# Kernel tuning notes

Hardware: AMD Instinct MI355X
Metric: run time of the kernel (lower is better)

Reference implementation:

```python
import jax, jax.numpy as jnp
import numpy as np

BS, S, D = 2, 2048, 1024
H = 16
DK = D // H  # 64
ROPE_BASE = 10000.0


def _rope(x):
    # x: [b, s, h, dk]; apply rotary embedding along s with per-pair angles.
    s, d = x.shape[1], x.shape[-1]
    theta = 1.0 / (ROPE_BASE ** (jnp.arange(0, d, 2, dtype=jnp.float32) / d))  # [d/2]
    ang = jnp.arange(s, dtype=jnp.float32)[:, None] * theta[None, :]            # [s, d/2]
    cos = jnp.cos(ang)[None, :, None, :]
    sin = jnp.sin(ang)[None, :, None, :]
    xs = x.reshape(*x.shape[:-1], d // 2, 2)
    x0, x1 = xs[..., 0], xs[..., 1]
    out = jnp.stack([x0 * cos - x1 * sin, x1 * cos + x0 * sin], axis=-1)
    return out.reshape(x.shape)


def setup_inputs() -> dict:
    key = jax.random.key(0)
    ks = jax.random.split(key, 7)
    w = 0.02
    return {
        "Q": jax.random.normal(ks[0], (BS, S, D), dtype=jnp.float32),
        "prev": jax.random.normal(ks[1], (BS, H, S, S), dtype=jnp.float32) * 0.1,
        "Wq": jax.random.normal(ks[2], (D, H * DK), dtype=jnp.float32) * w,
        "bq": jnp.zeros((H * DK,), dtype=jnp.float32),
        "Wk": jax.random.normal(ks[3], (D, H * DK), dtype=jnp.float32) * w,
        "bk": jnp.zeros((H * DK,), dtype=jnp.float32),
        "Wv": jax.random.normal(ks[4], (D, H * DK), dtype=jnp.float32) * w,
        "bv": jnp.zeros((H * DK,), dtype=jnp.float32),
        "Wo": jax.random.normal(ks[5], (H * DK, D), dtype=jnp.float32) * w,
        "bo": jnp.zeros((D,), dtype=jnp.float32),
    }


def reference(Q, prev, Wq, bq, Wk, bk, Wv, bv, Wo, bo):
    bs, s, _ = Q.shape
    scale = DK ** -0.5
    # QKV projections (self-attention: K = V = Q)
    q = (Q @ Wq + bq).reshape(bs, s, H, DK)
    k = (Q @ Wk + bk).reshape(bs, s, H, DK)
    v = (Q @ Wv + bv).reshape(bs, s, H, DK)
    # RoPE on q and k (per-call, matching the torch module)
    q = _rope(q)
    k = _rope(k)
    # scores with residual bias from previous layer
    attn_scores = jnp.einsum("bqhd,bkhd->bhqk", q, k) * scale + prev
    attn_weights = jax.nn.softmax(attn_scores, axis=-1)  # dropout p=0.0
    out = jnp.einsum("bhqk,bkhd->bqhd", attn_weights, v).reshape(bs, s, H * DK)
    out = out @ Wo + bo  # proj dropout p=0.0
    return out, attn_scores
```

## Files before the change

kernel.cpp:

```cpp
#include <hip/hip_runtime.h>
#include <hip/hip_bf16.h>
#include <math.h>
#include <cstdint>

#define S_LEN 2048
#define DKH 64

typedef __attribute__((ext_vector_type(8))) short s16x8;
typedef __attribute__((ext_vector_type(4))) float f32x4;

__device__ __forceinline__ unsigned short f2bf(float f) {
  unsigned int u = __float_as_uint(f);
  return (unsigned short)((u + 0x7fffu + ((u >> 16) & 1u)) >> 16);
}

__device__ __forceinline__ void glds16(const unsigned short* g, unsigned short* l) {
  __builtin_amdgcn_global_load_lds(
      (const __attribute__((address_space(1))) unsigned int*)(uintptr_t)g,
      (__attribute__((address_space(3))) unsigned int*)(uintptr_t)l, 16, 0, 0);
}

__global__ void k_rope_table(float* __restrict__ cosT, float* __restrict__ sinT) {
  int idx = blockIdx.x * 256 + threadIdx.x;
  if (idx >= S_LEN * 32) return;
  int s = idx >> 5, i = idx & 31;
  float theta = powf(10000.0f, -(float)i / 32.0f);
  float ang = (float)s * theta;
  float sv, cv;
  sincosf(ang, &sv, &cv);
  cosT[idx] = cv;
  sinT[idx] = sv;
}

__global__ __launch_bounds__(256) void k_wtrans(const float* __restrict__ W,
                                                unsigned short* __restrict__ WT) {
  __shared__ float t[32][33];
  int n0 = blockIdx.x * 32, k0 = blockIdx.y * 32;
  int tx = threadIdx.x & 31, ty = threadIdx.x >> 5;
#pragma unroll
  for (int p = 0; p < 4; ++p)
    t[ty + p * 8][tx] = W[(size_t)(k0 + ty + p * 8) * 1024 + n0 + tx];
  __syncthreads();
#pragma unroll
  for (int p = 0; p < 4; ++p)
    WT[(size_t)(n0 + ty + p * 8) * 1024 + k0 + tx] = f2bf(t[tx][ty + p * 8]);
}

__global__ __launch_bounds__(256) void k_qconv(const float* __restrict__ Q,
                                               unsigned short* __restrict__ Qbf) {
  int idx = (blockIdx.x * 256 + threadIdx.x) * 8;
  float4 a = *(const float4*)(Q + idx);
  float4 b = *(const float4*)(Q + idx + 4);
  s16x8 o;
  o[0] = (short)f2bf(a.x); o[1] = (short)f2bf(a.y); o[2] = (short)f2bf(a.z); o[3] = (short)f2bf(a.w);
  o[4] = (short)f2bf(b.x); o[5] = (short)f2bf(b.y); o[6] = (short)f2bf(b.z); o[7] = (short)f2bf(b.w);
  *(s16x8*)(Qbf + idx) = o;
}

__global__ __launch_bounds__(256) void k_vtrans(const unsigned short* __restrict__ vl,
                                                unsigned short* __restrict__ vt) {
  __shared__ unsigned short t[64][65];
  int bh = blockIdx.y;
  int s0 = blockIdx.x * 64;
  int tx = threadIdx.x & 3;
  int r = threadIdx.x >> 2;
  const unsigned short* src = vl + (size_t)bh * S_LEN * DKH + (size_t)s0 * DKH;
  s16x8 a = *(const s16x8*)(src + r * 64 + tx * 16);
  s16x8 b = *(const s16x8*)(src + r * 64 + tx * 16 + 8);
#pragma unroll
  for (int j = 0; j < 8; ++j) { t[r][tx * 16 + j] = (unsigned short)a[j]; t[r][tx * 16 + 8 + j] = (unsigned short)b[j]; }
  __syncthreads();
  unsigned short* dst = vt + (size_t)bh * DKH * S_LEN + (size_t)r * S_LEN + s0;
  s16x8 o0, o1;
#pragma unroll
  for (int j = 0; j < 8; ++j) { o0[j] = (short)t[tx * 16 + j][r]; o1[j] = (short)t[tx * 16 + 8 + j][r]; }
  *(s16x8*)(dst + tx * 16) = o0;
  *(s16x8*)(dst + tx * 16 + 8) = o1;
}

__global__ __launch_bounds__(256) void k_qkv(
    const unsigned short* __restrict__ Qbf, const unsigned short* __restrict__ WTqkv,
    const float* __restrict__ bq, const float* __restrict__ bk, const float* __restrict__ bv,
    const float* __restrict__ cosT, const float* __restrict__ sinT,
    unsigned short* __restrict__ ql, unsigned short* __restrict__ kl,
    unsigned short* __restrict__ vl) {
  __shared__ unsigned short As[128 * 64];
  __shared__ unsigned short Bs[128 * 64];
  const int m0 = blockIdx.y * 128, n0 = blockIdx.x * 128;
  const int tid = threadIdx.x, lane = tid & 63, wave = tid >> 6;
  const int wm = (wave >> 1) * 64, wn = (wave & 1) * 64;
  const int lr = lane & 15, lg = lane >> 4;
  const int widx = n0 >> 10;
  const float* bias = widx == 0 ? bq : (widx == 1 ? bk : bv);
  const int lrow = lane >> 3, lcol = (lane & 7) * 8;

  f32x4 acc[4][4] = {};
  for (int k0 = 0; k0 < 1024; k0 += 64) {
    __syncthreads();
#pragma unroll
    for (int i = 0; i < 4; ++i) {
      int chunk = wave * 4 + i;
      glds16(Qbf + (size_t)(m0 + 8 * chunk + lrow) * 1024 + k0 + lcol, &As[chunk * 512]);
      glds16(WTqkv + (size_t)(n0 + 8 * chunk + lrow) * 1024 + k0 + lcol, &Bs[chunk * 512]);
    }
    __syncthreads();
#pragma unroll
    for (int ks = 0; ks < 2; ++ks) {
      s16x8 af[4], bf[4];
#pragma unroll
      for (int i = 0; i < 4; ++i) af[i] = *(const s16x8*)&As[(wm + i * 16 + lr) * 64 + ks * 32 + lg * 8];
#pragma unroll
      for (int i = 0; i < 4; ++i) bf[i] = *(const s16x8*)&Bs[(wn + i * 16 + lr) * 64 + ks * 32 + lg * 8];
#pragma unroll
      for (int mi = 0; mi < 4; ++mi)
#pragma unroll
        for (int ni = 0; ni < 4; ++ni)
          acc[mi][ni] = __builtin_amdgcn_mfma_f32_16x16x32_bf16(af[mi], bf[ni], acc[mi][ni], 0, 0, 0);
    }
  }

#pragma unroll
  for (int ni = 0; ni < 4; ++ni) {
    int n = n0 + wn + ni * 16 + lr;
    int np = n & 1023;
    float bval = bias[np];
    int h = np >> 6, d = np & 63;
    int ia = d >> 1;
#pragma unroll
    for (int mi = 0; mi < 4; ++mi) {
#pragma unroll
      for (int r = 0; r < 4; ++r) {
        int m = m0 + wm + mi * 16 + lg * 4 + r;
        int s = m & 2047, b = m >> 11;
        float val = acc[mi][ni][r] + bval;
        size_t oidx = ((size_t)(b * 16 + h) * 2048 + s) * 64 + d;
        if (widx == 2) {
          vl[oidx] = f2bf(val);
        } else {
          float part = __shfl_xor(val, 1);
          float c = cosT[s * 32 + ia], sn = sinT[s * 32 + ia];
          float outv = (d & 1) ? (val * c + part * sn) : (val * c - part * sn);
          (widx == 0 ? ql : kl)[oidx] = f2bf(outv);
        }
      }
    }
  }
}

__global__ __launch_bounds__(256, 4) void k_attn(
    const unsigned short* __restrict__ ql, const unsigned short* __restrict__ kl,
    const unsigned short* __restrict__ vt, const float* __restrict__ prev,
    float* __restrict__ scores, unsigned short* __restrict__ attn_out) {
  __shared__ unsigned short Ks[2][64 * 64];
  __shared__ unsigned short Vs[2][64 * 64];
  __shared__ unsigned short Ps[4][16 * 64];

  const int bid = blockIdx.x;
  const int xcd = bid & 7, idx = bid >> 3;
  const int bh = xcd * 4 + (idx >> 5);
  const int qb = idx & 31;

  const int tid = threadIdx.x, lane = tid & 63, wave = tid >> 6;
  const int lr = lane & 15, lg = lane >> 4;
  const int qw = qb * 64 + wave * 16;
  const int kr = lane >> 3, kc = lane & 7;

  s16x8 qf[2];
#pragma unroll
  for (int ks = 0; ks < 2; ++ks)
    qf[ks] = *(const s16x8*)(ql + ((size_t)bh * S_LEN + qw + lr) * DKH + ks * 32 + lg * 8);

  f32x4 o[4] = {};
  float m_run[4], l_run[4];
#pragma unroll
  for (int r = 0; r < 4; ++r) { m_run[r] = -1e30f; l_run[r] = 0.f; }

  const float scale = 0.125f;
  const unsigned short* kbase = kl + (size_t)bh * S_LEN * DKH;
  const unsigned short* vbase = vt + (size_t)bh * DKH * S_LEN;
  const float* prevB = prev + (size_t)bh * S_LEN * S_LEN;
  float* scoB = scores + (size_t)bh * S_LEN * S_LEN;
  unsigned short* PsW = &Ps[wave][0];

#pragma unroll
  for (int half = 0; half < 2; ++half) {
    const int rb = wave * 16 + half * 8;
    const int row = rb + kr;
    glds16(kbase + (size_t)row * DKH + ((kc ^ kr) * 8), &Ks[0][rb * 64]);
    glds16(vbase + (size_t)row * S_LEN + ((kc ^ kr) * 8), &Vs[0][rb * 64]);
  }
  asm volatile("s_waitcnt vmcnt(0)" ::: "memory");
  __builtin_amdgcn_s_barrier();

  for (int t = 0; t < 32; ++t) {
    const int cur = t & 1;
    const int kv0 = t * 64;
    const int kvn = ((t + 1) & 31) * 64;

    float pvv[16];
#pragma unroll
    for (int n = 0; n < 4; ++n)
#pragma unroll
      for (int r = 0; r < 4; ++r)
        pvv[n * 4 + r] = __builtin_nontemporal_load(
            prevB + (size_t)(qw + lg * 4 + r) * S_LEN + kv0 + n * 16 + lr);
    __builtin_amdgcn_sched_barrier(0);

#pragma unroll
    for (int half = 0; half < 2; ++half) {
      const int rb = wave * 16 + half * 8;
      const int row = rb + kr;
      glds16(kbase + (size_t)(kvn + row) * DKH + ((kc ^ kr) * 8), &Ks[cur ^ 1][rb * 64]);
      glds16(vbase + (size_t)row * S_LEN + kvn + ((kc ^ kr) * 8), &Vs[cur ^ 1][rb * 64]);
    }
    __builtin_amdgcn_sched_barrier(0);

    f32x4 sc[4];
#pragma unroll
    for (int n = 0; n < 4; ++n) {
      f32x4 a = {};
#pragma unroll
      for (int ks = 0; ks < 2; ++ks) {
        s16x8 kf = *(const s16x8*)((const char*)&Ks[cur][0] + (n * 16 + lr) * 128 +
                                   ((ks * 64 + lg * 16) ^ ((lr & 7) << 4)));
        a = __builtin_amdgcn_mfma_f32_16x16x32_bf16(qf[ks], kf, a, 0, 0, 0);
      }
      sc[n] = a;
    }

    float tmax[4] = {-1e30f, -1e30f, -1e30f, -1e30f};
#pragma unroll
    for (int n = 0; n < 4; ++n) {
      const int col = kv0 + n * 16 + lr;
#pragma unroll
      for (int r = 0; r < 4; ++r) {
        float v = sc[n][r] * scale + pvv[n * 4 + r];
        __builtin_nontemporal_store(v, scoB + (size_t)(qw + lg * 4 + r) * S_LEN + col);
        sc[n][r] = v;
        tmax[r] = fmaxf(tmax[r], v);
      }
    }
#pragma unroll
    for (int mask = 1; mask < 16; mask <<= 1)
#pragma unroll
      for (int r = 0; r < 4; ++r) tmax[r] = fmaxf(tmax[r], __shfl_xor(tmax[r], mask));

#pragma unroll
    for (int r = 0; r < 4; ++r) {
      const float mn = fmaxf(m_run[r], tmax[r]);
      const float al = __expf(m_run[r] - mn);
      m_run[r] = mn;
      l_run[r] *= al;
#pragma unroll
      for (int df = 0; df < 4; ++df) o[df][r] *= al;
    }

#pragma unroll
    for (int n = 0; n < 4; ++n)
#pragma unroll
      for (int r = 0; r < 4; ++r) {
        const float p = __expf(sc[n][r] - m_run[r]);
        l_run[r] += p;
        const int prow = lg * 4 + r;
        *(unsigned short*)((char*)PsW + prow * 128 +
                           ((n * 32 + lr * 2) ^ ((prow & 7) << 4))) = f2bf(p);
      }

    s16x8 pa[2];
#pragma unroll
    for (int ks = 0; ks < 2; ++ks)
      pa[ks] = *(const s16x8*)((const char*)PsW + lr * 128 +
                               ((ks * 64 + lg * 16) ^ ((lr & 7) << 4)));
#pragma unroll
    for (int df = 0; df < 4; ++df) {
#pragma unroll
      for (int ks = 0; ks < 2; ++ks) {
        s16x8 vb = *(const s16x8*)((const char*)&Vs[cur][0] + (df * 16 + lr) * 128 +
                                   ((ks * 64 + lg * 16) ^ ((lr & 7) << 4)));
        o[df] = __builtin_amdgcn_mfma_f32_16x16x32_bf16(pa[ks], vb, o[df], 0, 0, 0);
      }
    }

    asm volatile("s_waitcnt vmcnt(16)" ::: "memory");
    __builtin_amdgcn_s_barrier();
  }

#pragma unroll
  for (int mask = 1; mask < 16; mask <<= 1)
#pragma unroll
    for (int r = 0; r < 4; ++r) l_run[r] += __shfl_xor(l_run[r], mask);
  float inv[4];
#pragma unroll
  for (int r = 0; r < 4; ++r) inv[r] = 1.0f / l_run[r];

  const int b = bh >> 4, h = bh & 15;
#pragma unroll
  for (int df = 0; df < 4; ++df) {
    const int d = df * 16 + lr;
#pragma unroll
    for (int r = 0; r < 4; ++r) {
      const int row = qw + lg * 4 + r;
      attn_out[((size_t)(b * S_LEN + row)) * 1024 + h * 64 + d] = f2bf(o[df][r] * inv[r]);
    }
  }
}

__global__ __launch_bounds__(256) void k_outproj(
    const unsigned short* __restrict__ A, const unsigned short* __restrict__ WoT,
    const float* __restrict__ bo, float* __restrict__ out) {
  __shared__ unsigned short As[128 * 64];
  __shared__ unsigned short Bs[128 * 64];
  const int m0 = blockIdx.y * 128, n0 = blockIdx.x * 128;
  const int tid = threadIdx.x, lane = tid & 63, wave = tid >> 6;
  const int wm = (wave >> 1) * 64, wn = (wave & 1) * 64;
  const int lr = lane & 15, lg = lane >> 4;
  const int lrow = lane >> 3, lcol = (lane & 7) * 8;
  f32x4 acc[4][4] = {};
  for (int k0 = 0; k0 < 1024; k0 += 64) {
    __syncthreads();
#pragma unroll
    for (int i = 0; i < 4; ++i) {
      int chunk = wave * 4 + i;
      glds16(A + (size_t)(m0 + 8 * chunk + lrow) * 1024 + k0 + lcol, &As[chunk * 512]);
      glds16(WoT + (size_t)(n0 + 8 * chunk + lrow) * 1024 + k0 + lcol, &Bs[chunk * 512]);
    }
    __syncthreads();
#pragma unroll
    for (int ks = 0; ks < 2; ++ks) {
      s16x8 af[4], bf[4];
#pragma unroll
      for (int i = 0; i < 4; ++i) af[i] = *(const s16x8*)&As[(wm + i * 16 + lr) * 64 + ks * 32 + lg * 8];
#pragma unroll
      for (int i = 0; i < 4; ++i) bf[i] = *(const s16x8*)&Bs[(wn + i * 16 + lr) * 64 + ks * 32 + lg * 8];
#pragma unroll
      for (int mi = 0; mi < 4; ++mi)
#pragma unroll
        for (int ni = 0; ni < 4; ++ni)
          acc[mi][ni] = __builtin_amdgcn_mfma_f32_16x16x32_bf16(af[mi], bf[ni], acc[mi][ni], 0, 0, 0);
    }
  }
#pragma unroll
  for (int ni = 0; ni < 4; ++ni) {
    int n = n0 + wn + ni * 16 + lr;
    float bv = bo[n];
#pragma unroll
    for (int mi = 0; mi < 4; ++mi)
#pragma unroll
      for (int rr = 0; rr < 4; ++rr) {
        int m = m0 + wm + mi * 16 + lg * 4 + rr;
        out[(size_t)m * 1024 + n] = acc[mi][ni][rr] + bv;
      }
  }
}

extern "C" void kernel_launch(void* const* d_in, const int* in_sizes, int n_in,
                              void* d_out, int out_size, void* d_ws, size_t ws_size,
                              hipStream_t stream) {
  const float* Q = (const float*)d_in[0];
  const float* prev = (const float*)d_in[1];
  const float* Wq = (const float*)d_in[2];
  const float* bq = (const float*)d_in[3];
  const float* Wk = (const float*)d_in[4];
  const float* bk = (const float*)d_in[5];
  const float* Wv = (const float*)d_in[6];
  const float* bv = (const float*)d_in[7];
  const float* Wo = (const float*)d_in[8];
  const float* bo = (const float*)d_in[9];

  float* out = (float*)d_out;
  float* scores = out + (size_t)4194304;

  char* ws = (char*)d_ws;
  float* cosT = (float*)ws;
  float* sinT = cosT + 65536;
  unsigned short* WTqkv = (unsigned short*)(ws + 524288);
  unsigned short* WoT = WTqkv + 3145728;
  unsigned short* ql = WoT + 1048576;
  unsigned short* kl = ql + 4194304;
  unsigned short* vl = kl + 4194304;
  unsigned short* vt = vl + 4194304;
  unsigned short* attn_out = vt + 4194304;
  unsigned short* Qbf = attn_out + 4194304;

  k_rope_table<<<256, 256, 0, stream>>>(cosT, sinT);
  k_wtrans<<<dim3(32, 32), 256, 0, stream>>>(Wq, WTqkv);
  k_wtrans<<<dim3(32, 32), 256, 0, stream>>>(Wk, WTqkv + 1048576);
  k_wtrans<<<dim3(32, 32), 256, 0, stream>>>(Wv, WTqkv + 2097152);
  k_wtrans<<<dim3(32, 32), 256, 0, stream>>>(Wo, WoT);
  k_qconv<<<2048, 256, 0, stream>>>(Q, Qbf);
  k_qkv<<<dim3(24, 32), 256, 0, stream>>>(Qbf, WTqkv, bq, bk, bv, cosT, sinT, ql, kl, vl);
  k_vtrans<<<dim3(32, 32), 256, 0, stream>>>(vl, vt);
  k_attn<<<1024, 256, 0, stream>>>(ql, kl, vt, prev, scores, attn_out);
  k_outproj<<<dim3(8, 32), 256, 0, stream>>>(attn_out, WoT, bo, out);
}
```

Before: 384.8 us.

## Widen attention KV tile, read V directly into registers, merge weight transposes, shrink outproj tiles

The attention kernel now processes 128 keys per iteration, which halves the loop trips and barriers. It drops the LDS staging of V and instead loads V fragments straight from global memory into registers, with occupancy lowered to 3 waves per SIMD. The four weight-transpose launches are merged into one 3D-grid kernel. The output projection moves to 64x64 tiles so more blocks run in parallel. The exchange is higher register pressure and uncoalesced per-wave global V reads that every wave repeats, with no LDS sharing of V.

Result: slower. 510.9 us (+32.8%).

```diff
diff --git a/kernel.cpp b/kernel.cpp
--- a/kernel.cpp
+++ b/kernel.cpp
@@ -14,7 +14,7 @@
   return (unsigned short)((u + 0x7fffu + ((u >> 16) & 1u)) >> 16);
 }
 
-__device__ __forceinline__ void glds16(const unsigned short* g, unsigned short* l) {
+__device__ __forceinline__ void glds16(const void* g, void* l) {
   __builtin_amdgcn_global_load_lds(
       (const __attribute__((address_space(1))) unsigned int*)(uintptr_t)g,
       (__attribute__((address_space(3))) unsigned int*)(uintptr_t)l, 16, 0, 0);
@@ -32,9 +32,14 @@
   sinT[idx] = sv;
 }
 
-__global__ __launch_bounds__(256) void k_wtrans(const float* __restrict__ W,
-                                                unsigned short* __restrict__ WT) {
+__global__ __launch_bounds__(256) void k_wtrans4(const float* __restrict__ W0,
+                                                 const float* __restrict__ W1,
+                                                 const float* __restrict__ W2,
+                                                 const float* __restrict__ W3,
+                                                 unsigned short* __restrict__ WT) {
   __shared__ float t[32][33];
+  const float* W = blockIdx.z == 0 ? W0 : (blockIdx.z == 1 ? W1 : (blockIdx.z == 2 ? W2 : W3));
+  unsigned short* dst = WT + (size_t)blockIdx.z * 1048576;
   int n0 = blockIdx.x * 32, k0 = blockIdx.y * 32;
   int tx = threadIdx.x & 31, ty = threadIdx.x >> 5;
 #pragma unroll
@@ -43,7 +48,7 @@
   __syncthreads();
 #pragma unroll
   for (int p = 0; p < 4; ++p)
-    WT[(size_t)(n0 + ty + p * 8) * 1024 + k0 + tx] = f2bf(t[tx][ty + p * 8]);
+    dst[(size_t)(n0 + ty + p * 8) * 1024 + k0 + tx] = f2bf(t[tx][ty + p * 8]);
 }
 
 __global__ __launch_bounds__(256) void k_qconv(const float* __restrict__ Q,
@@ -147,13 +152,12 @@
   }
 }
 
-__global__ __launch_bounds__(256, 4) void k_attn(
+__global__ __launch_bounds__(256, 3) void k_attn(
     const unsigned short* __restrict__ ql, const unsigned short* __restrict__ kl,
     const unsigned short* __restrict__ vt, const float* __restrict__ prev,
     float* __restrict__ scores, unsigned short* __restrict__ attn_out) {
-  __shared__ unsigned short Ks[2][64 * 64];
-  __shared__ unsigned short Vs[2][64 * 64];
-  __shared__ unsigned short Ps[4][16 * 64];
+  __shared__ unsigned short Ks[2][128 * 64];
+  __shared__ unsigned short Ps[4][16 * 128];
 
   const int bid = blockIdx.x;
   const int xcd = bid & 7, idx = bid >> 3;
@@ -183,23 +187,22 @@
   unsigned short* PsW = &Ps[wave][0];
 
 #pragma unroll
-  for (int half = 0; half < 2; ++half) {
-    const int rb = wave * 16 + half * 8;
+  for (int half = 0; half < 4; ++half) {
+    const int rb = wave * 32 + half * 8;
     const int row = rb + kr;
     glds16(kbase + (size_t)row * DKH + ((kc ^ kr) * 8), &Ks[0][rb * 64]);
-    glds16(vbase + (size_t)row * S_LEN + ((kc ^ kr) * 8), &Vs[0][rb * 64]);
   }
   asm volatile("s_waitcnt vmcnt(0)" ::: "memory");
   __builtin_amdgcn_s_barrier();
 
-  for (int t = 0; t < 32; ++t) {
+  for (int t = 0; t < 16; ++t) {
     const int cur = t & 1;
-    const int kv0 = t * 64;
-    const int kvn = ((t + 1) & 31) * 64;
-
-    float pvv[16];
-#pragma unroll
-    for (int n = 0; n < 4; ++n)
+    const int kv0 = t * 128;
+    const int kvn = ((t + 1) & 15) * 128;
+
+    float pvv[32];
+#pragma unroll
+    for (int n = 0; n < 8; ++n)
 #pragma unroll
       for (int r = 0; r < 4; ++r)
         pvv[n * 4 + r] = __builtin_nontemporal_load(
@@ -207,17 +210,25 @@
     __builtin_amdgcn_sched_barrier(0);
 
 #pragma unroll
-    for (int half = 0; half < 2; ++half) {
-      const int rb = wave * 16 + half * 8;
+    for (int half = 0; half < 4; ++half) {
+      const int rb = wave * 32 + half * 8;
       const int row = rb + kr;
       glds16(kbase + (size_t)(kvn + row) * DKH + ((kc ^ kr) * 8), &Ks[cur ^ 1][rb * 64]);
-      glds16(vbase + (size_t)row * S_LEN + kvn + ((kc ^ kr) * 8), &Vs[cur ^ 1][rb * 64]);
     }
     __builtin_amdgcn_sched_barrier(0);
 
-    f32x4 sc[4];
-#pragma unroll
-    for (int n = 0; n < 4; ++n) {
+    s16x8 vf1[8];
+#pragma unroll
+    for (int df = 0; df < 4; ++df)
+#pragma unroll
+      for (int ks = 0; ks < 2; ++ks)
+        vf1[df * 2 + ks] =
+            *(const s16x8*)(vbase + (size_t)(df * 16 + lr) * S_LEN + kv0 + ks * 32 + lg * 8);
+    __builtin_amdgcn_sched_barrier(0);
+
+    f32x4 sc[8];
+#pragma unroll
+    for (int n = 0; n < 8; ++n) {
       f32x4 a = {};
 #pragma unroll
       for (int ks = 0; ks < 2; ++ks) {
@@ -230,7 +241,7 @@
 
     float tmax[4] = {-1e30f, -1e30f, -1e30f, -1e30f};
 #pragma unroll
-    for (int n = 0; n < 4; ++n) {
+    for (int n = 0; n < 8; ++n) {
       const int col = kv0 + n * 16 + lr;
 #pragma unroll
       for (int r = 0; r < 4; ++r) {
@@ -240,6 +251,16 @@
         tmax[r] = fmaxf(tmax[r], v);
       }
     }
+
+    s16x8 vf2[8];
+#pragma unroll
+    for (int df = 0; df < 4; ++df)
+#pragma unroll
+      for (int ks = 0; ks < 2; ++ks)
+        vf2[df * 2 + ks] =
+            *(const s16x8*)(vbase + (size_t)(df * 16 + lr) * S_LEN + kv0 + (ks + 2) * 32 + lg * 8);
+    __builtin_amdgcn_sched_barrier(0);
+
 #pragma unroll
     for (int mask = 1; mask < 16; mask <<= 1)
 #pragma unroll
@@ -256,32 +277,29 @@
     }
 
 #pragma unroll
-    for (int n = 0; n < 4; ++n)
+    for (int n = 0; n < 8; ++n)
 #pragma unroll
       for (int r = 0; r < 4; ++r) {
         const float p = __expf(sc[n][r] - m_run[r]);
         l_run[r] += p;
         const int prow = lg * 4 + r;
-        *(unsigned short*)((char*)PsW + prow * 128 +
+        *(unsigned short*)((char*)PsW + prow * 256 +
                            ((n * 32 + lr * 2) ^ ((prow & 7) << 4))) = f2bf(p);
       }
 
-    s16x8 pa[2];
-#pragma unroll
-    for (int ks = 0; ks < 2; ++ks)
-      pa[ks] = *(const s16x8*)((const char*)PsW + lr * 128 +
+    s16x8 pa[4];
+#pragma unroll
+    for (int ks = 0; ks < 4; ++ks)
+      pa[ks] = *(const s16x8*)((const char*)PsW + lr * 256 +
                                ((ks * 64 + lg * 16) ^ ((lr & 7) << 4)));
 #pragma unroll
     for (int df = 0; df < 4; ++df) {
-#pragma unroll
-      for (int ks = 0; ks < 2; ++ks) {
-        s16x8 vb = *(const s16x8*)((const char*)&Vs[cur][0] + (df * 16 + lr) * 128 +
-                                   ((ks * 64 + lg * 16) ^ ((lr & 7) << 4)));
-        o[df] = __builtin_amdgcn_mfma_f32_16x16x32_bf16(pa[ks], vb, o[df], 0, 0, 0);
-      }
-    }
-
-    asm volatile("s_waitcnt vmcnt(16)" ::: "memory");
+      o[df] = __builtin_amdgcn_mfma_f32_16x16x32_bf16(pa[0], vf1[df * 2 + 0], o[df], 0, 0, 0);
+      o[df] = __builtin_amdgcn_mfma_f32_16x16x32_bf16(pa[1], vf1[df * 2 + 1], o[df], 0, 0, 0);
+      o[df] = __builtin_amdgcn_mfma_f32_16x16x32_bf16(pa[2], vf2[df * 2 + 0], o[df], 0, 0, 0);
+      o[df] = __builtin_amdgcn_mfma_f32_16x16x32_bf16(pa[3], vf2[df * 2 + 1], o[df], 0, 0, 0);
+    }
+
     __builtin_amdgcn_s_barrier();
   }
 
@@ -308,43 +326,43 @@
 __global__ __launch_bounds__(256) void k_outproj(
     const unsigned short* __restrict__ A, const unsigned short* __restrict__ WoT,
     const float* __restrict__ bo, float* __restrict__ out) {
-  __shared__ unsigned short As[128 * 64];
-  __shared__ unsigned short Bs[128 * 64];
-  const int m0 = blockIdx.y * 128, n0 = blockIdx.x * 128;
+  __shared__ unsigned short As[64 * 64];
+  __shared__ unsigned short Bs[64 * 64];
+  const int m0 = blockIdx.y * 64, n0 = blockIdx.x * 64;
   const int tid = threadIdx.x, lane = tid & 63, wave = tid >> 6;
-  const int wm = (wave >> 1) * 64, wn = (wave & 1) * 64;
+  const int wm = (wave >> 1) * 32, wn = (wave & 1) * 32;
   const int lr = lane & 15, lg = lane >> 4;
   const int lrow = lane >> 3, lcol = (lane & 7) * 8;
-  f32x4 acc[4][4] = {};
+  f32x4 acc[2][2] = {};
   for (int k0 = 0; k0 < 1024; k0 += 64) {
     __syncthreads();
 #pragma unroll
-    for (int i = 0; i < 4; ++i) {
-      int chunk = wave * 4 + i;
+    for (int i = 0; i < 2; ++i) {
+      int chunk = wave * 2 + i;
       glds16(A + (size_t)(m0 + 8 * chunk + lrow) * 1024 + k0 + lcol, &As[chunk * 512]);
       glds16(WoT + (size_t)(n0 + 8 * chunk + lrow) * 1024 + k0 + lcol, &Bs[chunk * 512]);
     }
     __syncthreads();
 #pragma unroll
     for (int ks = 0; ks < 2; ++ks) {
-      s16x8 af[4], bf[4];
-#pragma unroll
-      for (int i = 0; i < 4; ++i) af[i] = *(const s16x8*)&As[(wm + i * 16 + lr) * 64 + ks * 32 + lg * 8];
-#pragma unroll
-      for (int i = 0; i < 4; ++i) bf[i] = *(const s16x8*)&Bs[(wn + i * 16 + lr) * 64 + ks * 32 + lg * 8];
-#pragma unroll
-      for (int mi = 0; mi < 4; ++mi)
-#pragma unroll
-        for (int ni = 0; ni < 4; ++ni)
+      s16x8 af[2], bf[2];
+#pragma unroll
+      for (int i = 0; i < 2; ++i) af[i] = *(const s16x8*)&As[(wm + i * 16 + lr) * 64 + ks * 32 + lg * 8];
+#pragma unroll
+      for (int i = 0; i < 2; ++i) bf[i] = *(const s16x8*)&Bs[(wn + i * 16 + lr) * 64 + ks * 32 + lg * 8];
+#pragma unroll
+      for (int mi = 0; mi < 2; ++mi)
+#pragma unroll
+        for (int ni = 0; ni < 2; ++ni)
           acc[mi][ni] = __builtin_amdgcn_mfma_f32_16x16x32_bf16(af[mi], bf[ni], acc[mi][ni], 0, 0, 0);
     }
   }
 #pragma unroll
-  for (int ni = 0; ni < 4; ++ni) {
+  for (int ni = 0; ni < 2; ++ni) {
     int n = n0 + wn + ni * 16 + lr;
     float bv = bo[n];
 #pragma unroll
-    for (int mi = 0; mi < 4; ++mi)
+    for (int mi = 0; mi < 2; ++mi)
 #pragma unroll
       for (int rr = 0; rr < 4; ++rr) {
         int m = m0 + wm + mi * 16 + lg * 4 + rr;
@@ -383,13 +401,10 @@
   unsigned short* Qbf = attn_out + 4194304;
 
   k_rope_table<<<256, 256, 0, stream>>>(cosT, sinT);
-  k_wtrans<<<dim3(32, 32), 256, 0, stream>>>(Wq, WTqkv);
-  k_wtrans<<<dim3(32, 32), 256, 0, stream>>>(Wk, WTqkv + 1048576);
-  k_wtrans<<<dim3(32, 32), 256, 0, stream>>>(Wv, WTqkv + 2097152);
-  k_wtrans<<<dim3(32, 32), 256, 0, stream>>>(Wo, WoT);
+  k_wtrans4<<<dim3(32, 32, 4), 256, 0, stream>>>(Wq, Wk, Wv, Wo, WTqkv);
   k_qconv<<<2048, 256, 0, stream>>>(Q, Qbf);
   k_qkv<<<dim3(24, 32), 256, 0, stream>>>(Qbf, WTqkv, bq, bk, bv, cosT, sinT, ql, kl, vl);
   k_vtrans<<<dim3(32, 32), 256, 0, stream>>>(vl, vt);
   k_attn<<<1024, 256, 0, stream>>>(ql, kl, vt, prev, scores, attn_out);
-  k_outproj<<<dim3(8, 32), 256, 0, stream>>>(attn_out, WoT, bo, out);
-}
+  k_outproj<<<dim3(16, 64), 256, 0, stream>>>(attn_out, WoT, bo, out);
+}
```
